# Kernel tuning notes

Hardware: AMD Instinct MI355X
Metric: run time of the kernel (lower is better)

## Reference

```python
import jax, jax.numpy as jnp
import numpy as np

D_MODEL = 768
N_HEADS = 12
D_HEAD = 64
D_EMBED = N_HEADS * D_HEAD  # 768


def setup_inputs() -> dict:
    key = jax.random.key(0)
    ks = jax.random.split(key, 5)
    b, p = 2, 2048
    x = jax.random.normal(ks[0], (b, p, D_MODEL), dtype=jnp.float32)
    # nn.Linear default init scale ~ 1/sqrt(fan_in)
    Wqkv = jax.random.normal(ks[1], (D_MODEL, 3 * D_EMBED), dtype=jnp.float32) / np.sqrt(D_MODEL)
    bqkv = jax.random.normal(ks[2], (3 * D_EMBED,), dtype=jnp.float32) * 0.01
    Wout = jax.random.normal(ks[3], (D_EMBED, D_MODEL), dtype=jnp.float32) / np.sqrt(D_EMBED)
    bout = jax.random.normal(ks[4], (D_MODEL,), dtype=jnp.float32) * 0.01
    return {"x": x, "Wqkv": Wqkv, "bqkv": bqkv, "Wout": Wout, "bout": bout}


def reference(x, Wqkv, bqkv, Wout, bout):
    b, p, d = x.shape
    qkv = x @ Wqkv + bqkv                                   # [b, p, 3*D_EMBED]
    qkv = qkv.reshape(b, p, N_HEADS, 3 * D_HEAD).transpose(0, 2, 1, 3)  # [b, h, p, 3*dh]
    q, k, v = jnp.split(qkv, 3, axis=-1)                    # each [b, h, p, dh]
    # FAITHFUL to source bug: logits /= d_head**(-0.5)  ==  logits *= sqrt(d_head)
    logits = jnp.einsum('bhqd,bhkd->bhqk', q, k) * jnp.sqrt(jnp.float32(D_HEAD))
    attn = jax.nn.softmax(logits, axis=-1)                  # [b, h, p, p]
    out = jnp.einsum('bhqk,bhkd->bhqd', attn, v)            # [b, h, p, dh]
    out = out.transpose(0, 2, 1, 3).reshape(b, p, D_EMBED)  # [b, p, D_EMBED]
    return out @ Wout + bout                                # [b, p, D_MODEL]
```

## Files before the change

kernel.cpp:

```cpp
#include <hip/hip_runtime.h>
#include <stdint.h>

#define LOG2E 1.44269504088896340736f

typedef __bf16 v8bf __attribute__((ext_vector_type(8)));
typedef _Float16 v8h __attribute__((ext_vector_type(8)));
typedef float f32x4 __attribute__((ext_vector_type(4)));
typedef float f32x16 __attribute__((ext_vector_type(16)));
typedef unsigned int v4u __attribute__((ext_vector_type(4)));
typedef unsigned int v2u __attribute__((ext_vector_type(2)));

__device__ __forceinline__ unsigned short f2bf(float f) {
  union { float f; uint32_t u; } v; v.f = f;
  uint32_t u = v.u;
  uint32_t r = (u + 0x7FFFu + ((u >> 16) & 1u)) >> 16;
  return (unsigned short)r;
}
__device__ __forceinline__ void gll16(const void* g, void* l) {
  __builtin_amdgcn_global_load_lds(
      (const __attribute__((address_space(1))) unsigned int*)g,
      (__attribute__((address_space(3))) unsigned int*)l, 16, 0, 0);
}
__device__ __forceinline__ uint32_t pk2(float a, float b) {
  union { __bf16 h[2]; uint32_t u; } x;
  x.h[0] = (__bf16)a; x.h[1] = (__bf16)b;
  return x.u;
}


__global__ void prep_fused(const float* __restrict__ x, const float* __restrict__ Wqkv,
                           const float* __restrict__ Wout,
                           _Float16* __restrict__ Ah,
                           _Float16* __restrict__ Whk,
                           _Float16* __restrict__ Wv,
                           unsigned short* __restrict__ WoT) {
  const int t = threadIdx.x, f = blockIdx.x;
  if (f < 12288) {
    int m = f / 3, n = (f - m * 3) * 256 + t;
    Ah[(size_t)m * 768 + n] = (_Float16)x[(size_t)m * 768 + n];
  } else if (f < 19200) {
    int g = f - 12288;
    int cp = g / 3, k = (g - cp * 3) * 256 + t;
    int n;
    if (cp < 1536) n = (cp >> 7) * 192 + (cp & 127);
    else           n = ((cp - 1536) >> 6) * 192 + 128 + ((cp - 1536) & 63);
    float v = Wqkv[(size_t)k * 2304 + n];
    if (cp < 1536) Whk[(size_t)cp * 768 + k] = (_Float16)v;
    else           Wv[(size_t)(cp - 1536) * 768 + k] = (_Float16)v;
  } else {
    int g = f - 19200;
    int n = g / 3, k = (g - n * 3) * 256 + t;
    WoT[(size_t)n * 768 + k] = f2bf(Wout[(size_t)k * 768 + n]);
  }
}

__global__ __launch_bounds__(256) void gemm_qkv(
    const _Float16* __restrict__ Ah, const _Float16* __restrict__ Whk,
    const _Float16* __restrict__ Wv, const float* __restrict__ bqkv,
    _Float16* __restrict__ Qh, _Float16* __restrict__ Kh,
    unsigned short* __restrict__ VT) {
  __shared__ _Float16 As[128 * 32];
  __shared__ _Float16 Bs[128 * 32];
  const int t = threadIdx.x, f = blockIdx.x;
  const int w = t >> 6, l = t & 63, lr = l & 15, lg = l >> 4;
  const int wm = (w >> 1) * 64, wn = (w & 1) * 64;
  f32x4 acc[4][4] = {};

  if (f < 384) {
    const int xcd = f & 7, s = f >> 3;
    const int m0 = (xcd * 4 + (s & 3)) * 128;
    const int xt = s >> 2;
    const _Float16* Ap = Ah + (size_t)m0 * 768;
    const _Float16* Bp = Whk + (size_t)xt * 128 * 768;
    for (int kt = 0; kt < 24; ++kt) {
      const int k0 = kt << 5;
      const int c0 = t, c1 = t + 256;
      gll16(Ap + (size_t)(c0 >> 2) * 768 + k0 + ((c0 & 3) << 3), &As[c0 * 8]);
      gll16(Ap + (size_t)(c1 >> 2) * 768 + k0 + ((c1 & 3) << 3), &As[c1 * 8]);
      gll16(Bp + (size_t)(c0 >> 2) * 768 + k0 + ((c0 & 3) << 3), &Bs[c0 * 8]);
      gll16(Bp + (size_t)(c1 >> 2) * 768 + k0 + ((c1 & 3) << 3), &Bs[c1 * 8]);
      __syncthreads();
      v8h a[4], b[4];
#pragma unroll
      for (int i = 0; i < 4; i++) {
        a[i] = *(const v8h*)&As[(wm + i * 16 + lr) * 32 + lg * 8];
        b[i] = *(const v8h*)&Bs[(wn + i * 16 + lr) * 32 + lg * 8];
      }
#pragma unroll
      for (int i = 0; i < 4; i++)
#pragma unroll
        for (int j = 0; j < 4; j++)
          acc[i][j] = __builtin_amdgcn_mfma_f32_16x16x32_f16(a[i], b[j], acc[i][j], 0, 0, 0);
      __syncthreads();
    }
#pragma unroll
    for (int j = 0; j < 4; j++) {
      const int jj = j * 16 + lr;
      const float bv = bqkv[xt * 192 + wn + jj];
#pragma unroll
      for (int i = 0; i < 4; i++) {
#pragma unroll
        for (int r = 0; r < 4; r++) {
          const int m = m0 + wm + i * 16 + lg * 4 + r;
          const int b = m >> 11, p = m & 2047;
          size_t base = ((size_t)(b * 12 + xt) * 2048 + p) * 64;
          float val = acc[i][j][r] + bv;
          if (wn == 0) Qh[base + jj] = (_Float16)(val * (8.0f * LOG2E));
          else         Kh[base + jj] = (_Float16)val;
        }
      }
    }
  } else {
    const int g = f - 384;
    const int xcd = g & 7, s = g >> 3;
    const int m0v = (xcd * 4 + (s & 3)) * 128;
    const int d0 = (s >> 2) * 128;
    for (int kt = 0; kt < 24; ++kt) {
      const int k0 = kt << 5;
      const int c0 = t, c1 = t + 256;
      gll16(Wv + (size_t)(d0 + (c0 >> 2)) * 768 + k0 + ((c0 & 3) << 3), &As[c0 * 8]);
      gll16(Wv + (size_t)(d0 + (c1 >> 2)) * 768 + k0 + ((c1 & 3) << 3), &As[c1 * 8]);
      gll16(Ah + (size_t)(m0v + (c0 >> 2)) * 768 + k0 + ((c0 & 3) << 3), &Bs[c0 * 8]);
      gll16(Ah + (size_t)(m0v + (c1 >> 2)) * 768 + k0 + ((c1 & 3) << 3), &Bs[c1 * 8]);
      __syncthreads();
      v8h a[4], b[4];
#pragma unroll
      for (int i = 0; i < 4; i++) {
        a[i] = *(const v8h*)&As[(wm + i * 16 + lr) * 32 + lg * 8];
        b[i] = *(const v8h*)&Bs[(wn + i * 16 + lr) * 32 + lg * 8];
      }
#pragma unroll
      for (int i = 0; i < 4; i++)
#pragma unroll
        for (int j = 0; j < 4; j++)
          acc[i][j] = __builtin_amdgcn_mfma_f32_16x16x32_f16(a[i], b[j], acc[i][j], 0, 0, 0);
      __syncthreads();
    }
#pragma unroll
    for (int i = 0; i < 4; i++) {
#pragma unroll
      for (int r = 0; r < 4; r++) {
        const int drow = d0 + wm + i * 16 + lg * 4 + r;
        const int h = drow >> 6, dd = drow & 63;
        const float bv = bqkv[h * 192 + 128 + dd];
#pragma unroll
        for (int j = 0; j < 4; j++) {
          const int m = m0v + wn + j * 16 + lr;
          const int b = m >> 11, p = m & 2047;
          VT[((size_t)(b * 12 + h) * 64 + dd) * 2048 + p] = f2bf(acc[i][j][r] + bv);
        }
      }
    }
  }
}

__global__ __launch_bounds__(256) void gemm_out(
    const unsigned short* __restrict__ A, const unsigned short* __restrict__ B,
    const float* __restrict__ bias, float* __restrict__ C) {
  __shared__ unsigned short As[64 * 32];
  __shared__ unsigned short Bs[128 * 32];
  const int t = threadIdx.x, f = blockIdx.x;
  const int xcd = f & 7, s = f >> 3;
  const int m0 = (xcd * 8 + (s & 7)) * 64;
  const int n0 = (s >> 3) * 128;
  const int w = t >> 6, l = t & 63, lr = l & 15, lg = l >> 4;
  const int wm = (w >> 1) * 32, wn = (w & 1) * 64;
  f32x4 acc[2][4] = {};
  for (int kt = 0; kt < 24; ++kt) {
    const int k0 = kt << 5;
    gll16(A + (size_t)(m0 + (t >> 2)) * 768 + k0 + ((t & 3) << 3), &As[t * 8]);
    gll16(B + (size_t)(n0 + (t >> 2)) * 768 + k0 + ((t & 3) << 3), &Bs[t * 8]);
    gll16(B + (size_t)(n0 + 64 + (t >> 2)) * 768 + k0 + ((t & 3) << 3), &Bs[(t + 256) * 8]);
    __syncthreads();
    v8bf a[2], b[4];
#pragma unroll
    for (int i = 0; i < 2; i++)
      a[i] = *(const v8bf*)&As[(wm + i * 16 + lr) * 32 + lg * 8];
#pragma unroll
    for (int j = 0; j < 4; j++)
      b[j] = *(const v8bf*)&Bs[(wn + j * 16 + lr) * 32 + lg * 8];
#pragma unroll
    for (int i = 0; i < 2; i++)
#pragma unroll
      for (int j = 0; j < 4; j++)
        acc[i][j] = __builtin_amdgcn_mfma_f32_16x16x32_bf16(a[i], b[j], acc[i][j], 0, 0, 0);
    __syncthreads();
  }
#pragma unroll
  for (int i = 0; i < 2; i++) {
#pragma unroll
    for (int j = 0; j < 4; j++) {
      const int col = n0 + wn + j * 16 + lr;
      const float bv = bias[col];
#pragma unroll
      for (int r = 0; r < 4; r++) {
        const int row = m0 + wm + i * 16 + lg * 4 + r;
        C[(size_t)row * 768 + col] = acc[i][j][r] + bv;
      }
    }
  }
}

__global__ __launch_bounds__(256, 4) void attn(
    const _Float16* __restrict__ Qh, const _Float16* __restrict__ Kh,
    const unsigned short* __restrict__ VT,
    __bf16* __restrict__ Op, float* __restrict__ Ml) {
  __shared__ __align__(16) _Float16 Ks[2][32 * 64];
  __shared__ __align__(16) unsigned short Vs[2][64 * 32];
  __shared__ float Al[4][32];
  const int t = threadIdx.x, w = t >> 6, l = t & 63;
  const int lq = l & 31, hi = l >> 5;
  const int f = blockIdx.x;
  const int xcd = f & 7, slot = f >> 3;
  const int p = xcd + 8 * (slot >> 4);
  const int bh = p >> 2, zsplit = p & 3;
  const int q0 = (slot & 15) * 128;
  const int qw0 = q0 + w * 32;
  const int NKT = 16;
  const int ktBase = zsplit * 16;
  const _Float16* Qb = Qh + (size_t)bh * 2048 * 64;
  const _Float16* Kb = Kh + (size_t)bh * 2048 * 64;
  const unsigned short* Vb = VT + (size_t)bh * 64 * 2048;

  const int krow = t >> 3, kpart = t & 7;
  const int kwofs = (krow * 64 + kpart * 8) ^ ((krow & 7) << 3);
  const int vd = t >> 2, vpart = t & 3;
  const int vwofs = (vd * 32 + vpart * 8) ^ ((vd & 3) << 3);

  const char* gK = (const char*)Kb + (size_t)ktBase * 4096 + (size_t)t * 16;
  const char* gV = (const char*)Vb + (size_t)vd * 4096 + (size_t)vpart * 16
                   + (size_t)ktBase * 64;

  v4u kreg, vreg;
  kreg = *(const v4u*)gK;
  vreg = *(const v4u*)gV;
  *(v4u*)&Ks[0][kwofs] = kreg;
  *(v4u*)&Vs[0][vwofs] = vreg;
  gK += 4096; gV += 64;
  kreg = *(const v4u*)gK;
  vreg = *(const v4u*)gV;

  v8h qf[4];
#pragma unroll
  for (int ks = 0; ks < 4; ++ks)
    qf[ks] = *(const v8h*)(Qb + (size_t)(qw0 + lq) * 64 + ks * 16 + hi * 8);

  f32x16 o0 = {}, o1 = {};
  float mrun = -1e30f, lsum = 0.f;
  const int sxk = (lq & 7) << 3;
  const int sxv = (lq & 3) << 3;
  __syncthreads();

  for (int kt = 0; kt < NKT; ++kt) {
    const _Float16* ksb = &Ks[kt & 1][0];
    const unsigned short* vsb = &Vs[kt & 1][0];
    _Float16* ksw = &Ks[(kt & 1) ^ 1][0];
    unsigned short* vsw = &Vs[(kt & 1) ^ 1][0];

    f32x16 s = {};
    __builtin_amdgcn_s_setprio(1);
#pragma unroll
    for (int ks = 0; ks < 4; ++ks) {
      v8h ka = *(const v8h*)&ksb[(lq * 64 + ks * 16 + hi * 8) ^ sxk];
      s = __builtin_amdgcn_mfma_f32_32x32x16_f16(ka, qf[ks], s, 0, 0, 0);
    }
    __builtin_amdgcn_s_setprio(0);

    if (kt < NKT - 1) {
      *(v4u*)&ksw[kwofs] = kreg;
      *(v4u*)&vsw[vwofs] = vreg;
    }
    if (kt < NKT - 2) {
      gK += 4096; gV += 64;
      kreg = *(const v4u*)gK;
      vreg = *(const v4u*)gV;
    }

    float tm[8];
#pragma unroll
    for (int i = 0; i < 8; i++) tm[i] = fmaxf(s[i], s[i + 8]);
#pragma unroll
    for (int i = 0; i < 4; i++) tm[i] = fmaxf(tm[i], tm[i + 4]);
    float pmax = fmaxf(fmaxf(tm[0], tm[1]), fmaxf(tm[2], tm[3]));
    {
      v2u r = __builtin_amdgcn_permlane32_swap(__float_as_uint(pmax),
                                               __float_as_uint(pmax), false, false);
      pmax = fmaxf(__uint_as_float(r.x), __uint_as_float(r.y));
    }

    if (__any(pmax > mrun + 32.f)) {
      float mnew = fmaxf(mrun, pmax);
      float a = __builtin_exp2f(mrun - mnew);
      mrun = mnew;
      lsum *= a;
      if (!hi) Al[w][lq] = a;
#pragma unroll
      for (int r = 0; r < 16; r++) {
        float ar = Al[w][(r & 3) + 8 * (r >> 2) + 4 * hi];
        o0[r] *= ar; o1[r] *= ar;
      }
    }

#pragma unroll
    for (int i = 0; i < 16; i++) s[i] = __builtin_exp2f(s[i] - mrun);
    {
      float a0 = (s[0] + s[8]) + (s[1] + s[9]);
      float a1 = (s[2] + s[10]) + (s[3] + s[11]);
      float a2 = (s[4] + s[12]) + (s[5] + s[13]);
      float a3 = (s[6] + s[14]) + (s[7] + s[15]);
      float ps = (a0 + a1) + (a2 + a3);
      v2u r = __builtin_amdgcn_permlane32_swap(__float_as_uint(ps),
                                               __float_as_uint(ps), false, false);
      lsum += __uint_as_float(r.x) + __uint_as_float(r.y);
    }
    uint32_t paw[2][4];
    {
      v2u r0 = __builtin_amdgcn_permlane32_swap(pk2(s[0], s[1]), pk2(s[4], s[5]), false, false);
      v2u r1 = __builtin_amdgcn_permlane32_swap(pk2(s[2], s[3]), pk2(s[6], s[7]), false, false);
      paw[0][0] = r0.x; paw[0][2] = r0.y; paw[0][1] = r1.x; paw[0][3] = r1.y;
      v2u r2 = __builtin_amdgcn_permlane32_swap(pk2(s[8], s[9]), pk2(s[12], s[13]), false, false);
      v2u r3 = __builtin_amdgcn_permlane32_swap(pk2(s[10], s[11]), pk2(s[14], s[15]), false, false);
      paw[1][0] = r2.x; paw[1][2] = r2.y; paw[1][1] = r3.x; paw[1][3] = r3.y;
    }

    __builtin_amdgcn_s_setprio(1);
#pragma unroll
    for (int ks = 0; ks < 2; ++ks) {
      union { uint32_t u[4]; v8bf v; } pa;
      pa.u[0] = paw[ks][0]; pa.u[1] = paw[ks][1];
      pa.u[2] = paw[ks][2]; pa.u[3] = paw[ks][3];
      v8bf v0 = *(const v8bf*)&vsb[(lq * 32 + ks * 16 + hi * 8) ^ sxv];
      v8bf v1 = *(const v8bf*)&vsb[((lq + 32) * 32 + ks * 16 + hi * 8) ^ sxv];
      o0 = __builtin_amdgcn_mfma_f32_32x32x16_bf16(pa.v, v0, o0, 0, 0, 0);
      o1 = __builtin_amdgcn_mfma_f32_32x32x16_bf16(pa.v, v1, o1, 0, 0, 0);
    }
    __builtin_amdgcn_s_setprio(0);
    if (kt < NKT - 1) __syncthreads();
  }

  const size_t S = (size_t)24 * 2048;
  const size_t srow = (size_t)zsplit * S + (size_t)bh * 2048;
  if (!hi) {
    Ml[(srow + qw0 + lq) * 2]     = mrun;
    Ml[(srow + qw0 + lq) * 2 + 1] = lsum;
  }
#pragma unroll
  for (int r = 0; r < 16; r++) {
    const int q = qw0 + (r & 3) + 8 * (r >> 2) + 4 * hi;
    Op[(srow + q) * 64 + lq]      = (__bf16)o0[r];
    Op[(srow + q) * 64 + 32 + lq] = (__bf16)o1[r];
  }
}

__global__ __launch_bounds__(256) void attn_combine(
    const __bf16* __restrict__ Op, const float* __restrict__ Ml,
    __bf16* __restrict__ Oe) {
  const size_t S = (size_t)24 * 2048;
  int row = blockIdx.x * 4 + (threadIdx.x >> 6);
  int lane = threadIdx.x & 63;
  int bh = row >> 11, q = row & 2047;
  int b = bh / 12, h = bh - b * 12;
  float m[4], lv[4];
#pragma unroll
  for (int s = 0; s < 4; s++) {
    m[s]  = Ml[(s * S + row) * 2];
    lv[s] = Ml[(s * S + row) * 2 + 1];
  }
  float M = fmaxf(fmaxf(m[0], m[1]), fmaxf(m[2], m[3]));
  float num = 0.f, den = 0.f;
#pragma unroll
  for (int s = 0; s < 4; s++) {
    float a = __builtin_exp2f(m[s] - M);
    den += lv[s] * a;
    num += (float)Op[(s * S + row) * 64 + lane] * a;
  }
  Oe[((size_t)(b * 2048 + q)) * 768 + h * 64 + lane] = (__bf16)(num / den);
}

extern "C" void kernel_launch(void* const* d_in, const int* in_sizes, int n_in,
                              void* d_out, int out_size, void* d_ws, size_t ws_size,
                              hipStream_t stream) {
  const float* x    = (const float*)d_in[0];
  const float* Wqkv = (const float*)d_in[1];
  const float* bqkv = (const float*)d_in[2];
  const float* Wout = (const float*)d_in[3];
  const float* bout = (const float*)d_in[4];
  float* out = (float*)d_out;
  char* ws = (char*)d_ws;

  _Float16*       Ah    = (_Float16*)(ws + 0);
  _Float16*       Whk   = (_Float16*)(ws + 18874368);
  _Float16*       Wv    = (_Float16*)(ws + 25952256);
  _Float16*       Qh    = (_Float16*)(ws + 67239936);
  _Float16*       Kh    = (_Float16*)(ws + 86114304);
  unsigned short* VT    = (unsigned short*)(ws + 104988672);
  unsigned short* Oemb  = (unsigned short*)(ws + 111280128);
  unsigned short* WoT   = (unsigned short*)(ws + 117571584);
  __bf16*         Opart = (__bf16*)(ws + 0);
  float*          Mlpart= (float*)(ws + 52428800);

  prep_fused<<<dim3(21504), 256, 0, stream>>>(x, Wqkv, Wout, Ah, Whk, Wv, WoT);
  gemm_qkv<<<dim3(576), 256, 0, stream>>>(Ah, Whk, Wv, bqkv, Qh, Kh, VT);
  attn<<<dim3(1536), 256, 0, stream>>>(Qh, Kh, VT, Opart, Mlpart);
  attn_combine<<<dim3(12288), 256, 0, stream>>>(Opart, Mlpart, (__bf16*)Oemb);
  gemm_out<<<dim3(384), 256, 0, stream>>>(Oemb, WoT, bout, out);
}
```

Baseline: 137.2 us.

## Vectorize prep conversions and halve QKV GEMM tile to double block count

The prep kernel now converts eight elements per thread, using float4 loads for x and 16-byte stores for the transposed fp16/bf16 weights, which cuts the block count and the number of scalar stores. The QKV GEMM uses 64x128 tiles instead of 128x128, giving twice as many blocks for better occupancy and CU coverage on the MI355X. The trade-off is less data reuse per block and more redundant loads of the B operand. In the weight-transpose paths the strided column reads stay scalar and uncoalesced.

```diff
diff --git a/kernel.cpp b/kernel.cpp
--- a/kernel.cpp
+++ b/kernel.cpp
@@ -35,22 +35,33 @@
                            _Float16* __restrict__ Wv,
                            unsigned short* __restrict__ WoT) {
   const int t = threadIdx.x, f = blockIdx.x;
-  if (f < 12288) {
-    int m = f / 3, n = (f - m * 3) * 256 + t;
-    Ah[(size_t)m * 768 + n] = (_Float16)x[(size_t)m * 768 + n];
-  } else if (f < 19200) {
-    int g = f - 12288;
-    int cp = g / 3, k = (g - cp * 3) * 256 + t;
+  if (f < 1536) {
+    size_t idx = ((size_t)f * 256 + t) * 8;
+    float4 a = *(const float4*)(x + idx);
+    float4 b = *(const float4*)(x + idx + 4);
+    _Float16 h[8] = {(_Float16)a.x, (_Float16)a.y, (_Float16)a.z, (_Float16)a.w,
+                     (_Float16)b.x, (_Float16)b.y, (_Float16)b.z, (_Float16)b.w};
+    *(v4u*)(Ah + idx) = *(v4u*)h;
+  } else if (f < 2400) {
+    int gi = (f - 1536) * 256 + t;
+    int cp = gi / 96, k8 = (gi - cp * 96) * 8;
     int n;
     if (cp < 1536) n = (cp >> 7) * 192 + (cp & 127);
     else           n = ((cp - 1536) >> 6) * 192 + 128 + ((cp - 1536) & 63);
-    float v = Wqkv[(size_t)k * 2304 + n];
-    if (cp < 1536) Whk[(size_t)cp * 768 + k] = (_Float16)v;
-    else           Wv[(size_t)(cp - 1536) * 768 + k] = (_Float16)v;
+    _Float16 h[8];
+#pragma unroll
+    for (int i = 0; i < 8; i++)
+      h[i] = (_Float16)Wqkv[(size_t)(k8 + i) * 2304 + n];
+    if (cp < 1536) *(v4u*)(Whk + (size_t)cp * 768 + k8) = *(v4u*)h;
+    else           *(v4u*)(Wv + (size_t)(cp - 1536) * 768 + k8) = *(v4u*)h;
   } else {
-    int g = f - 19200;
-    int n = g / 3, k = (g - n * 3) * 256 + t;
-    WoT[(size_t)n * 768 + k] = f2bf(Wout[(size_t)k * 768 + n]);
+    int gi = (f - 2400) * 256 + t;
+    int n = gi / 96, k8 = (gi - n * 96) * 8;
+    unsigned short h[8];
+#pragma unroll
+    for (int i = 0; i < 8; i++)
+      h[i] = f2bf(Wout[(size_t)(k8 + i) * 768 + n]);
+    *(v4u*)(WoT + (size_t)n * 768 + k8) = *(v4u*)h;
   }
 }
 
@@ -59,35 +70,34 @@
     const _Float16* __restrict__ Wv, const float* __restrict__ bqkv,
     _Float16* __restrict__ Qh, _Float16* __restrict__ Kh,
     unsigned short* __restrict__ VT) {
-  __shared__ _Float16 As[128 * 32];
+  __shared__ _Float16 As[64 * 32];
   __shared__ _Float16 Bs[128 * 32];
   const int t = threadIdx.x, f = blockIdx.x;
   const int w = t >> 6, l = t & 63, lr = l & 15, lg = l >> 4;
-  const int wm = (w >> 1) * 64, wn = (w & 1) * 64;
-  f32x4 acc[4][4] = {};
-
-  if (f < 384) {
+  const int wm = (w >> 1) * 32, wn = (w & 1) * 64;
+  f32x4 acc[2][4] = {};
+
+  if (f < 768) {
     const int xcd = f & 7, s = f >> 3;
-    const int m0 = (xcd * 4 + (s & 3)) * 128;
-    const int xt = s >> 2;
+    const int m0 = (xcd * 8 + (s & 7)) * 64;
+    const int xt = s >> 3;
     const _Float16* Ap = Ah + (size_t)m0 * 768;
     const _Float16* Bp = Whk + (size_t)xt * 128 * 768;
     for (int kt = 0; kt < 24; ++kt) {
       const int k0 = kt << 5;
-      const int c0 = t, c1 = t + 256;
-      gll16(Ap + (size_t)(c0 >> 2) * 768 + k0 + ((c0 & 3) << 3), &As[c0 * 8]);
-      gll16(Ap + (size_t)(c1 >> 2) * 768 + k0 + ((c1 & 3) << 3), &As[c1 * 8]);
-      gll16(Bp + (size_t)(c0 >> 2) * 768 + k0 + ((c0 & 3) << 3), &Bs[c0 * 8]);
-      gll16(Bp + (size_t)(c1 >> 2) * 768 + k0 + ((c1 & 3) << 3), &Bs[c1 * 8]);
+      gll16(Ap + (size_t)(t >> 2) * 768 + k0 + ((t & 3) << 3), &As[t * 8]);
+      gll16(Bp + (size_t)(t >> 2) * 768 + k0 + ((t & 3) << 3), &Bs[t * 8]);
+      gll16(Bp + (size_t)(64 + (t >> 2)) * 768 + k0 + ((t & 3) << 3), &Bs[(t + 256) * 8]);
       __syncthreads();
-      v8h a[4], b[4];
-#pragma unroll
-      for (int i = 0; i < 4; i++) {
+      v8h a[2], b[4];
+#pragma unroll
+      for (int i = 0; i < 2; i++)
         a[i] = *(const v8h*)&As[(wm + i * 16 + lr) * 32 + lg * 8];
-        b[i] = *(const v8h*)&Bs[(wn + i * 16 + lr) * 32 + lg * 8];
-      }
-#pragma unroll
-      for (int i = 0; i < 4; i++)
+#pragma unroll
+      for (int j = 0; j < 4; j++)
+        b[j] = *(const v8h*)&Bs[(wn + j * 16 + lr) * 32 + lg * 8];
+#pragma unroll
+      for (int i = 0; i < 2; i++)
 #pragma unroll
         for (int j = 0; j < 4; j++)
           acc[i][j] = __builtin_amdgcn_mfma_f32_16x16x32_f16(a[i], b[j], acc[i][j], 0, 0, 0);
@@ -98,7 +108,7 @@
       const int jj = j * 16 + lr;
       const float bv = bqkv[xt * 192 + wn + jj];
 #pragma unroll
-      for (int i = 0; i < 4; i++) {
+      for (int i = 0; i < 2; i++) {
 #pragma unroll
         for (int r = 0; r < 4; r++) {
           const int m = m0 + wm + i * 16 + lg * 4 + r;
@@ -111,33 +121,32 @@
       }
     }
   } else {
-    const int g = f - 384;
+    const int g = f - 768;
     const int xcd = g & 7, s = g >> 3;
     const int m0v = (xcd * 4 + (s & 3)) * 128;
-    const int d0 = (s >> 2) * 128;
+    const int d0 = (s >> 2) * 64;
     for (int kt = 0; kt < 24; ++kt) {
       const int k0 = kt << 5;
-      const int c0 = t, c1 = t + 256;
-      gll16(Wv + (size_t)(d0 + (c0 >> 2)) * 768 + k0 + ((c0 & 3) << 3), &As[c0 * 8]);
-      gll16(Wv + (size_t)(d0 + (c1 >> 2)) * 768 + k0 + ((c1 & 3) << 3), &As[c1 * 8]);
-      gll16(Ah + (size_t)(m0v + (c0 >> 2)) * 768 + k0 + ((c0 & 3) << 3), &Bs[c0 * 8]);
-      gll16(Ah + (size_t)(m0v + (c1 >> 2)) * 768 + k0 + ((c1 & 3) << 3), &Bs[c1 * 8]);
+      gll16(Wv + (size_t)(d0 + (t >> 2)) * 768 + k0 + ((t & 3) << 3), &As[t * 8]);
+      gll16(Ah + (size_t)(m0v + (t >> 2)) * 768 + k0 + ((t & 3) << 3), &Bs[t * 8]);
+      gll16(Ah + (size_t)(m0v + 64 + (t >> 2)) * 768 + k0 + ((t & 3) << 3), &Bs[(t + 256) * 8]);
       __syncthreads();
-      v8h a[4], b[4];
-#pragma unroll
-      for (int i = 0; i < 4; i++) {
+      v8h a[2], b[4];
+#pragma unroll
+      for (int i = 0; i < 2; i++)
         a[i] = *(const v8h*)&As[(wm + i * 16 + lr) * 32 + lg * 8];
-        b[i] = *(const v8h*)&Bs[(wn + i * 16 + lr) * 32 + lg * 8];
-      }
-#pragma unroll
-      for (int i = 0; i < 4; i++)
+#pragma unroll
+      for (int j = 0; j < 4; j++)
+        b[j] = *(const v8h*)&Bs[(wn + j * 16 + lr) * 32 + lg * 8];
+#pragma unroll
+      for (int i = 0; i < 2; i++)
 #pragma unroll
         for (int j = 0; j < 4; j++)
           acc[i][j] = __builtin_amdgcn_mfma_f32_16x16x32_f16(a[i], b[j], acc[i][j], 0, 0, 0);
       __syncthreads();
     }
 #pragma unroll
-    for (int i = 0; i < 4; i++) {
+    for (int i = 0; i < 2; i++) {
 #pragma unroll
       for (int r = 0; r < 4; r++) {
         const int drow = d0 + wm + i * 16 + lg * 4 + r;
@@ -399,8 +408,8 @@
   __bf16*         Opart = (__bf16*)(ws + 0);
   float*          Mlpart= (float*)(ws + 52428800);
 
-  prep_fused<<<dim3(21504), 256, 0, stream>>>(x, Wqkv, Wout, Ah, Whk, Wv, WoT);
-  gemm_qkv<<<dim3(576), 256, 0, stream>>>(Ah, Whk, Wv, bqkv, Qh, Kh, VT);
+  prep_fused<<<dim3(2688), 256, 0, stream>>>(x, Wqkv, Wout, Ah, Whk, Wv, WoT);
+  gemm_qkv<<<dim3(1152), 256, 0, stream>>>(Ah, Whk, Wv, bqkv, Qh, Kh, VT);
   attn<<<dim3(1536), 256, 0, stream>>>(Qh, Kh, VT, Opart, Mlpart);
   attn_combine<<<dim3(12288), 256, 0, stream>>>(Opart, Mlpart, (__bf16*)Oemb);
   gemm_out<<<dim3(384), 256, 0, stream>>>(Oemb, WoT, bout, out);
```

Measured after the change: 142.5 us. +3.9%, slower.
